# Performance work log

Hardware: AMD Instinct MI355X
Metric: run time of the kernel (lower is better)

Reference implementation:

```python
import jax, jax.numpy as jnp
import numpy as np

N_NODES = 50000


def _gcn_norm(edge_index, num_nodes):
    # Add self-loops, then symmetric normalization deg^-1/2 A_hat deg^-1/2
    loop = jnp.arange(num_nodes, dtype=edge_index.dtype)
    src = jnp.concatenate([edge_index[0], loop])  # source j
    dst = jnp.concatenate([edge_index[1], loop])  # target i
    ones = jnp.ones(dst.shape[0], dtype=jnp.float32)
    deg = jax.ops.segment_sum(ones, dst, num_segments=num_nodes)
    dinv = jnp.where(deg > 0, jax.lax.rsqrt(deg), 0.0)
    norm = dinv[src] * dinv[dst]  # [E + N]
    return src, dst, norm


def _gcn_layer(x, src, dst, norm, W, b, num_nodes):
    h = x @ W                              # [N, out]
    m = h[src] * norm[:, None]             # gather + scale, [E+N, out]
    out = jax.ops.segment_sum(m, dst, num_segments=num_nodes)  # scatter-add
    return out + b


def setup_inputs() -> dict:
    key = jax.random.key(0)
    ks = jax.random.split(key, 8)
    d = 128
    E = 800000
    x = jax.random.normal(ks[0], (N_NODES, d), dtype=jnp.float32)
    edge_index = jax.random.randint(ks[1], (2, E), 0, N_NODES, dtype=jnp.int64)
    s = 1.0 / np.sqrt(d)
    W0 = jax.random.normal(ks[2], (d, d), dtype=jnp.float32) * s
    W1 = jax.random.normal(ks[3], (d, d), dtype=jnp.float32) * s
    W2 = jax.random.normal(ks[4], (d, d), dtype=jnp.float32) * s
    b0 = jnp.zeros((d,), dtype=jnp.float32)
    b1 = jnp.zeros((d,), dtype=jnp.float32)
    b2 = jnp.zeros((d,), dtype=jnp.float32)
    return {"x": x, "edge_index": edge_index, "W0": W0, "b0": b0,
            "W1": W1, "b1": b1, "W2": W2, "b2": b2}


def reference(x, edge_index, W0, b0, W1, b1, W2, b2):
    src, dst, norm = _gcn_norm(edge_index, N_NODES)
    for W, b in ((W0, b0), (W1, b1), (W2, b2)):  # k = 3 layers
        x = _gcn_layer(x, src, dst, norm, W, b, N_NODES)
        x = jax.nn.relu(x)
    return x
```

## Files before the change

kernel.cpp:

```cpp
#include <hip/hip_runtime.h>
#include <hip/hip_fp16.h>

#define D 128
#define BIN_CH 8192
#define CAP 6144

typedef _Float16 f16x4 __attribute__((ext_vector_type(4)));
typedef float f32x4 __attribute__((ext_vector_type(4)));

__global__ __launch_bounds__(256) void k_init(const int* __restrict__ ei32,
        const float* __restrict__ W0, const float* __restrict__ W1,
        const float* __restrict__ W2, int* __restrict__ flag,
        int* __restrict__ bcur, __half* __restrict__ Wt) {
    if (blockIdx.x == 0) {
        __shared__ int nz;
        if (threadIdx.x == 0) nz = 0;
        __syncthreads();
        int c = 0;
        for (int i = threadIdx.x; i < 1024; i += blockDim.x) {
            if (ei32[2 * i + 1] != 0) c++;
        }
        atomicAdd(&nz, c);
        bcur[threadIdx.x] = threadIdx.x * CAP;
        __syncthreads();
        if (threadIdx.x == 0) *flag = (nz == 0) ? 1 : 0;
        return;
    }
    int bb = blockIdx.x - 1;
    int which = bb >> 4;
    const float* W = (which == 0) ? W0 : (which == 1) ? W1 : W2;
    __half* dst = Wt + (size_t)which * D * D;
    int tid = (bb & 15) * 256 + threadIdx.x;
    int c  = tid >> 5;
    int k4 = (tid & 31) * 4;
    float w0 = W[(k4 + 0) * D + c];
    float w1 = W[(k4 + 1) * D + c];
    float w2 = W[(k4 + 2) * D + c];
    float w3 = W[(k4 + 3) * D + c];
    union { __half2 h2[2]; uint2 u; } pk;
    pk.h2[0] = __floats2half2_rn(w0, w1);
    pk.h2[1] = __floats2half2_rn(w2, w3);
    *(uint2*)&dst[(size_t)c * D + k4] = pk.u;
}

__device__ __forceinline__ int e_src(const void* ei, int e, int is64, int E) {
    return is64 ? (int)((const long long*)ei)[e] : ((const int*)ei)[e];
}
__device__ __forceinline__ int e_dst(const void* ei, int e, int is64, int E) {
    return is64 ? (int)((const long long*)ei)[E + e] : ((const int*)ei)[E + e];
}

__global__ __launch_bounds__(256) void k_binning(const void* __restrict__ ei, int E,
        const int* __restrict__ flag, int* __restrict__ bcur, int2* __restrict__ ebuck) {
    __shared__ int lcnt[256];
    __shared__ int lbase[256];
    int is64 = *flag;
    int t = threadIdx.x;
    int e0 = blockIdx.x * BIN_CH;
    int e1 = min(e0 + BIN_CH, E);
    lcnt[t] = 0;
    __syncthreads();
    for (int e = e0 + t; e < e1; e += 256) {
        int d = e_dst(ei, e, is64, E);
        atomicAdd(&lcnt[d >> 8], 1);
    }
    __syncthreads();
    int c = lcnt[t];
    if (c > 0) lbase[t] = atomicAdd(&bcur[t], c);
    __syncthreads();
    lcnt[t] = 0;
    __syncthreads();
    for (int e = e0 + t; e < e1; e += 256) {
        int s = e_src(ei, e, is64, E);
        int d = e_dst(ei, e, is64, E);
        int b = d >> 8;
        int idx = atomicAdd(&lcnt[b], 1);
        ebuck[lbase[b] + idx] = make_int2(s, d);
    }
}

__global__ __launch_bounds__(256) void k_bucket_build(const int2* __restrict__ ebuck,
        const int* __restrict__ bcur, int* __restrict__ row_start,
        unsigned short* __restrict__ deg, float* __restrict__ dinv,
        int* __restrict__ esrc, int N) {
    __shared__ int lcnt[256];
    __shared__ int sc[256];
    __shared__ int lbase2[256];
    int b = blockIdx.x;
    int t = threadIdx.x;
    int lo = b * CAP;
    int hi = bcur[b];
    lcnt[t] = 0;
    __syncthreads();
    for (int j = lo + t; j < hi; j += 256) {
        atomicAdd(&lcnt[ebuck[j].y & 255], 1);
    }
    __syncthreads();
    int cntv = lcnt[t];
    sc[t] = cntv;
    __syncthreads();
#pragma unroll
    for (int d = 1; d < 256; d <<= 1) {
        int tv = (t >= d) ? sc[t - d] : 0;
        __syncthreads();
        sc[t] += tv;
        __syncthreads();
    }
    lbase2[t] = lo + sc[t] - cntv;
    int node = (b << 8) + t;
    if (node < N) {
        row_start[node] = lbase2[t];
        deg[node] = (unsigned short)cntv;
        dinv[node] = rsqrtf((float)(cntv + 1));
    }
    lcnt[t] = 0;
    __syncthreads();
    for (int j = lo + t; j < hi; j += 256) {
        int2 ed = ebuck[j];
        int c = ed.y & 255;
        int idx = atomicAdd(&lcnt[c], 1);
        esrc[lbase2[c] + idx] = ed.x;
    }
}

template<bool IN16>
__global__ __launch_bounds__(256) void k_gemm_mfma(const void* __restrict__ xin,
        const __half* __restrict__ Wt, const float* __restrict__ dinv,
        __half* __restrict__ h, int N) {
    __shared__ __align__(16) char Ab[128 * 256];
    __shared__ __align__(16) char Bb[128 * 256];
    int t = threadIdx.x;
    int br = blockIdx.x * 128;

#pragma unroll
    for (int i = 0; i < 8; ++i) {
        int byte = (i * 256 + t) * 16;
        int c = byte >> 8;
        uint4 v = *(const uint4*)((const char*)Wt + byte);
        *(uint4*)(Bb + (byte ^ ((c & 7) << 4))) = v;
    }
    if (IN16) {
        const char* xp = (const char*)xin;
#pragma unroll
        for (int i = 0; i < 8; ++i) {
            int byte = (i * 256 + t) * 16;
            int row = byte >> 8;
            int gr = br + row;
            int co = byte & 255;
            uint4 v = make_uint4(0, 0, 0, 0);
            if (gr < N) {
                int chunk = co >> 6;
                v = *(const uint4*)(xp + (size_t)chunk * N * 64 + (size_t)gr * 64 + (co & 63));
            }
            *(uint4*)(Ab + (byte ^ ((row & 7) << 4))) = v;
        }
    } else {
        const float* xp = (const float*)xin;
#pragma unroll
        for (int i = 0; i < 16; ++i) {
            int fid = i * 256 + t;
            int row = fid >> 5;
            int col4 = (fid & 31) * 4;
            int gr = br + row;
            float4 v = make_float4(0.f, 0.f, 0.f, 0.f);
            if (gr < N) v = *(const float4*)&xp[(size_t)gr * D + col4];
            union { __half2 h2[2]; uint2 u; } pk;
            pk.h2[0] = __floats2half2_rn(v.x, v.y);
            pk.h2[1] = __floats2half2_rn(v.z, v.w);
            int byte = row * 256 + col4 * 2;
            *(uint2*)(Ab + (byte ^ ((row & 7) << 4))) = pk.u;
        }
    }
    __syncthreads();

    int w = t >> 6;
    int l = t & 63;
    int lrow = l & 15;
    int g = l >> 4;
    f32x4 acc[2][8] = {};
    int arow0 = w * 32 + lrow;
    int arow1 = arow0 + 16;
#pragma unroll
    for (int ks = 0; ks < 8; ++ks) {
        int kb = ks * 32 + g * 8;
        f16x4 a0 = *(const f16x4*)(Ab + ((arow0 * 256 + kb) ^ ((arow0 & 7) << 4)));
        f16x4 a1 = *(const f16x4*)(Ab + ((arow1 * 256 + kb) ^ ((arow1 & 7) << 4)));
#pragma unroll
        for (int nj = 0; nj < 8; ++nj) {
            int bc = nj * 16 + lrow;
            f16x4 b = *(const f16x4*)(Bb + ((bc * 256 + kb) ^ ((bc & 7) << 4)));
            acc[0][nj] = __builtin_amdgcn_mfma_f32_16x16x16f16(a0, b, acc[0][nj], 0, 0, 0);
            acc[1][nj] = __builtin_amdgcn_mfma_f32_16x16x16f16(a1, b, acc[1][nj], 0, 0, 0);
        }
    }
#pragma unroll
    for (int mi = 0; mi < 2; ++mi) {
        int rbase = br + w * 32 + mi * 16 + g * 4;
#pragma unroll
        for (int r = 0; r < 4; ++r) {
            int gr = rbase + r;
            if (gr < N) {
                float sc = dinv[gr];
#pragma unroll
                for (int nj = 0; nj < 8; ++nj) {
                    size_t idx = (size_t)(nj >> 1) * N * 32 + (size_t)gr * 32
                               + (nj & 1) * 16 + lrow;
                    h[idx] = __float2half(acc[mi][nj][r] * sc);
                }
            }
        }
    }
}

__device__ __forceinline__ void acc_row(uint4 u, float* a) {
    float2 q;
    q = __half22float2(*(const __half2*)&u.x); a[0] += q.x; a[1] += q.y;
    q = __half22float2(*(const __half2*)&u.y); a[2] += q.x; a[3] += q.y;
    q = __half22float2(*(const __half2*)&u.z); a[4] += q.x; a[5] += q.y;
    q = __half22float2(*(const __half2*)&u.w); a[6] += q.x; a[7] += q.y;
}

template<int WRITE_F32>
__global__ __launch_bounds__(256) void k_agg(const __half* __restrict__ h,
        const int* __restrict__ row_start, const unsigned short* __restrict__ deg,
        const int* __restrict__ esrc, const float* __restrict__ dinv,
        const float* __restrict__ bias, float* __restrict__ out,
        __half* __restrict__ act, int N) {
    int xcd   = blockIdx.x & 7;
    int chunk = xcd >> 1;
    int rank  = ((blockIdx.x >> 3) << 1) + (xcd & 1);
    int node = rank * 64 + (threadIdx.x >> 2);
    int l4 = threadIdx.x & 3;
    if (node >= N) return;
    float di = dinv[node];
    const uint4* hv = (const uint4*)(h + (size_t)chunk * N * 32);
    int j0 = row_start[node];
    int j1 = j0 + deg[node];

    float a[8] = {};
    acc_row(hv[(size_t)node * 4 + l4], a);

    int j = j0;
    for (; j + 8 <= j1; j += 8) {
        int s0 = esrc[j],     s1 = esrc[j + 1], s2 = esrc[j + 2], s3 = esrc[j + 3];
        int s4 = esrc[j + 4], s5 = esrc[j + 5], s6 = esrc[j + 6], s7 = esrc[j + 7];
        uint4 u0 = hv[(size_t)s0 * 4 + l4];
        uint4 u1 = hv[(size_t)s1 * 4 + l4];
        uint4 u2 = hv[(size_t)s2 * 4 + l4];
        uint4 u3 = hv[(size_t)s3 * 4 + l4];
        uint4 u4 = hv[(size_t)s4 * 4 + l4];
        uint4 u5 = hv[(size_t)s5 * 4 + l4];
        uint4 u6 = hv[(size_t)s6 * 4 + l4];
        uint4 u7 = hv[(size_t)s7 * 4 + l4];
        acc_row(u0, a); acc_row(u1, a); acc_row(u2, a); acc_row(u3, a);
        acc_row(u4, a); acc_row(u5, a); acc_row(u6, a); acc_row(u7, a);
    }
    for (; j + 4 <= j1; j += 4) {
        int s0 = esrc[j], s1 = esrc[j + 1], s2 = esrc[j + 2], s3 = esrc[j + 3];
        uint4 u0 = hv[(size_t)s0 * 4 + l4];
        uint4 u1 = hv[(size_t)s1 * 4 + l4];
        uint4 u2 = hv[(size_t)s2 * 4 + l4];
        uint4 u3 = hv[(size_t)s3 * 4 + l4];
        acc_row(u0, a); acc_row(u1, a); acc_row(u2, a); acc_row(u3, a);
    }
    for (; j < j1; ++j) {
        acc_row(hv[(size_t)esrc[j] * 4 + l4], a);
    }
    const float4* b4 = (const float4*)bias;
    float4 bv0 = b4[chunk * 8 + l4 * 2], bv1 = b4[chunk * 8 + l4 * 2 + 1];
    float o[8];
    o[0] = fmaxf(fmaf(a[0], di, bv0.x), 0.f);
    o[1] = fmaxf(fmaf(a[1], di, bv0.y), 0.f);
    o[2] = fmaxf(fmaf(a[2], di, bv0.z), 0.f);
    o[3] = fmaxf(fmaf(a[3], di, bv0.w), 0.f);
    o[4] = fmaxf(fmaf(a[4], di, bv1.x), 0.f);
    o[5] = fmaxf(fmaf(a[5], di, bv1.y), 0.f);
    o[6] = fmaxf(fmaf(a[6], di, bv1.z), 0.f);
    o[7] = fmaxf(fmaf(a[7], di, bv1.w), 0.f);
    if (WRITE_F32) {
        float4* o4 = (float4*)out;
        o4[(size_t)node * 32 + chunk * 8 + l4 * 2]     = make_float4(o[0], o[1], o[2], o[3]);
        o4[(size_t)node * 32 + chunk * 8 + l4 * 2 + 1] = make_float4(o[4], o[5], o[6], o[7]);
    } else {
        union { __half2 h2[4]; uint4 u; } pk;
        pk.h2[0] = __floats2half2_rn(o[0], o[1]);
        pk.h2[1] = __floats2half2_rn(o[2], o[3]);
        pk.h2[2] = __floats2half2_rn(o[4], o[5]);
        pk.h2[3] = __floats2half2_rn(o[6], o[7]);
        ((uint4*)act)[(size_t)chunk * N * 4 + (size_t)node * 4 + l4] = pk.u;
    }
}

extern "C" void kernel_launch(void* const* d_in, const int* in_sizes, int n_in,
                              void* d_out, int out_size, void* d_ws, size_t ws_size,
                              hipStream_t stream) {
    const float* x  = (const float*)d_in[0];
    const void*  ei = d_in[1];
    const float* W0 = (const float*)d_in[2];
    const float* b0 = (const float*)d_in[3];
    const float* W1 = (const float*)d_in[4];
    const float* b1 = (const float*)d_in[5];
    const float* W2 = (const float*)d_in[6];
    const float* b2 = (const float*)d_in[7];
    float* out = (float*)d_out;

    const int N = in_sizes[0] / D;
    const int E = in_sizes[1] / 2;

    char* ws = (char*)d_ws;
    size_t off = 0;
    auto alloc = [&](size_t bytes) {
        char* p = ws + off;
        off = (off + bytes + 255) & ~(size_t)255;
        return p;
    };
    int*            flag      = (int*)alloc(4);
    int*            bcur      = (int*)alloc(256 * 4);
    int*            row_start = (int*)alloc((size_t)N * 4);
    unsigned short* deg       = (unsigned short*)alloc((size_t)N * 2);
    float*          dinv      = (float*)alloc((size_t)N * 4);
    int*            esrc      = (int*)alloc((size_t)256 * CAP * 4);
    __half*         hbuf      = (__half*)alloc((size_t)N * D * 2);
    __half*         act       = (__half*)alloc((size_t)N * D * 2);
    __half*         Wt        = (__half*)alloc((size_t)3 * D * D * 2);
    int2*           ebuck     = (int2*)hbuf;
    (void)ws_size;

    const int nbuck = (N + 255) >> 8;
    const int nbin  = (E + BIN_CH - 1) / BIN_CH;

    k_init<<<49, 256, 0, stream>>>((const int*)ei, W0, W1, W2, flag, bcur, Wt);
    k_binning<<<nbin, 256, 0, stream>>>(ei, E, flag, bcur, ebuck);
    k_bucket_build<<<nbuck, 256, 0, stream>>>(ebuck, bcur, row_start, deg, dinv, esrc, N);

    const int gemm_grid = (N + 127) / 128;
    const int ranks     = (N + 63) / 64;
    const int aggB      = (((ranks + 1) / 2)) * 8;

    k_gemm_mfma<false><<<gemm_grid, 256, 0, stream>>>(x, Wt, dinv, hbuf, N);
    k_agg<0><<<aggB, 256, 0, stream>>>(hbuf, row_start, deg, esrc, dinv, b0, out, act, N);
    k_gemm_mfma<true><<<gemm_grid, 256, 0, stream>>>(act, Wt + (size_t)D * D, dinv, hbuf, N);
    k_agg<0><<<aggB, 256, 0, stream>>>(hbuf, row_start, deg, esrc, dinv, b1, out, act, N);
    k_gemm_mfma<true><<<gemm_grid, 256, 0, stream>>>(act, Wt + (size_t)2 * D * D, dinv, hbuf, N);
    k_agg<1><<<aggB, 256, 0, stream>>>(hbuf, row_start, deg, esrc, dinv, b2, out, act, N);
}
```

Baseline: 176.8 us.

## Sort nodes by degree so aggregation warps process similar-degree nodes

```diff
diff --git a/kernel.cpp b/kernel.cpp
--- a/kernel.cpp
+++ b/kernel.cpp
@@ -11,7 +11,7 @@
 __global__ __launch_bounds__(256) void k_init(const int* __restrict__ ei32,
         const float* __restrict__ W0, const float* __restrict__ W1,
         const float* __restrict__ W2, int* __restrict__ flag,
-        int* __restrict__ bcur, __half* __restrict__ Wt) {
+        int* __restrict__ bcur, int* __restrict__ dhist, __half* __restrict__ Wt) {
     if (blockIdx.x == 0) {
         __shared__ int nz;
         if (threadIdx.x == 0) nz = 0;
@@ -22,6 +22,7 @@
         }
         atomicAdd(&nz, c);
         bcur[threadIdx.x] = threadIdx.x * CAP;
+        dhist[threadIdx.x] = 0;
         __syncthreads();
         if (threadIdx.x == 0) *flag = (nz == 0) ? 1 : 0;
         return;
@@ -82,7 +83,7 @@
 __global__ __launch_bounds__(256) void k_bucket_build(const int2* __restrict__ ebuck,
         const int* __restrict__ bcur, int* __restrict__ row_start,
         unsigned short* __restrict__ deg, float* __restrict__ dinv,
-        int* __restrict__ esrc, int N) {
+        int* __restrict__ esrc, int* __restrict__ dhist, int N) {
     __shared__ int lcnt[256];
     __shared__ int sc[256];
     __shared__ int lbase2[256];
@@ -112,6 +113,7 @@
         row_start[node] = lbase2[t];
         deg[node] = (unsigned short)cntv;
         dinv[node] = rsqrtf((float)(cntv + 1));
+        atomicAdd(&dhist[min(cntv, 255)], 1);
     }
     lcnt[t] = 0;
     __syncthreads();
@@ -121,6 +123,32 @@
         int idx = atomicAdd(&lcnt[c], 1);
         esrc[lbase2[c] + idx] = ed.x;
     }
+}
+
+__global__ __launch_bounds__(256) void k_deg_scan(const int* __restrict__ dhist,
+                                                  int* __restrict__ dcur) {
+    __shared__ int sh[256];
+    int t = threadIdx.x;
+    int v = dhist[t];
+    sh[t] = v;
+    __syncthreads();
+#pragma unroll
+    for (int d = 1; d < 256; d <<= 1) {
+        int tv = (t >= d) ? sh[t - d] : 0;
+        __syncthreads();
+        sh[t] += tv;
+        __syncthreads();
+    }
+    dcur[t] = sh[t] - v;
+}
+
+__global__ __launch_bounds__(256) void k_deg_scatter(const unsigned short* __restrict__ deg,
+        int* __restrict__ dcur, int* __restrict__ order, int N) {
+    int node = blockIdx.x * 256 + threadIdx.x;
+    if (node >= N) return;
+    int dv = min((int)deg[node], 255);
+    int pos = atomicAdd(&dcur[dv], 1);
+    order[pos] = node;
 }
 
 template<bool IN16>
@@ -223,15 +251,16 @@
 template<int WRITE_F32>
 __global__ __launch_bounds__(256) void k_agg(const __half* __restrict__ h,
         const int* __restrict__ row_start, const unsigned short* __restrict__ deg,
-        const int* __restrict__ esrc, const float* __restrict__ dinv,
-        const float* __restrict__ bias, float* __restrict__ out,
-        __half* __restrict__ act, int N) {
+        const int* __restrict__ esrc, const int* __restrict__ order,
+        const float* __restrict__ dinv, const float* __restrict__ bias,
+        float* __restrict__ out, __half* __restrict__ act, int N) {
     int xcd   = blockIdx.x & 7;
     int chunk = xcd >> 1;
     int rank  = ((blockIdx.x >> 3) << 1) + (xcd & 1);
-    int node = rank * 64 + (threadIdx.x >> 2);
+    int idx = rank * 64 + (threadIdx.x >> 2);
     int l4 = threadIdx.x & 3;
-    if (node >= N) return;
+    if (idx >= N) return;
+    int node = order[idx];
     float di = dinv[node];
     const uint4* hv = (const uint4*)(h + (size_t)chunk * N * 32);
     int j0 = row_start[node];
@@ -316,9 +345,12 @@
     };
     int*            flag      = (int*)alloc(4);
     int*            bcur      = (int*)alloc(256 * 4);
+    int*            dhist     = (int*)alloc(256 * 4);
+    int*            dcur      = (int*)alloc(256 * 4);
     int*            row_start = (int*)alloc((size_t)N * 4);
     unsigned short* deg       = (unsigned short*)alloc((size_t)N * 2);
     float*          dinv      = (float*)alloc((size_t)N * 4);
+    int*            order     = (int*)alloc((size_t)N * 4);
     int*            esrc      = (int*)alloc((size_t)256 * CAP * 4);
     __half*         hbuf      = (__half*)alloc((size_t)N * D * 2);
     __half*         act       = (__half*)alloc((size_t)N * D * 2);
@@ -329,18 +361,20 @@
     const int nbuck = (N + 255) >> 8;
     const int nbin  = (E + BIN_CH - 1) / BIN_CH;
 
-    k_init<<<49, 256, 0, stream>>>((const int*)ei, W0, W1, W2, flag, bcur, Wt);
+    k_init<<<49, 256, 0, stream>>>((const int*)ei, W0, W1, W2, flag, bcur, dhist, Wt);
     k_binning<<<nbin, 256, 0, stream>>>(ei, E, flag, bcur, ebuck);
-    k_bucket_build<<<nbuck, 256, 0, stream>>>(ebuck, bcur, row_start, deg, dinv, esrc, N);
+    k_bucket_build<<<nbuck, 256, 0, stream>>>(ebuck, bcur, row_start, deg, dinv, esrc, dhist, N);
+    k_deg_scan<<<1, 256, 0, stream>>>(dhist, dcur);
+    k_deg_scatter<<<nbuck, 256, 0, stream>>>(deg, dcur, order, N);
 
     const int gemm_grid = (N + 127) / 128;
     const int ranks     = (N + 63) / 64;
     const int aggB      = (((ranks + 1) / 2)) * 8;
 
     k_gemm_mfma<false><<<gemm_grid, 256, 0, stream>>>(x, Wt, dinv, hbuf, N);
-    k_agg<0><<<aggB, 256, 0, stream>>>(hbuf, row_start, deg, esrc, dinv, b0, out, act, N);
+    k_agg<0><<<aggB, 256, 0, stream>>>(hbuf, row_start, deg, esrc, order, dinv, b0, out, act, N);
     k_gemm_mfma<true><<<gemm_grid, 256, 0, stream>>>(act, Wt + (size_t)D * D, dinv, hbuf, N);
-    k_agg<0><<<aggB, 256, 0, stream>>>(hbuf, row_start, deg, esrc, dinv, b1, out, act, N);
+    k_agg<0><<<aggB, 256, 0, stream>>>(hbuf, row_start, deg, esrc, order, dinv, b1, out, act, N);
     k_gemm_mfma<true><<<gemm_grid, 256, 0, stream>>>(act, Wt + (size_t)2 * D * D, dinv, hbuf, N);
-    k_agg<1><<<aggB, 256, 0, stream>>>(hbuf, row_start, deg, esrc, dinv, b2, out, act, N);
-}
+    k_agg<1><<<aggB, 256, 0, stream>>>(hbuf, row_start, deg, esrc, order, dinv, b2, out, act, N);
+}
```

New measurement: 458.0 us. 2.59x slower.
